# Performance work log

Measured on AMD Instinct MI355X. Metric: run time of the kernel, lower is better.

The kernel has to match this reference:

```python
import jax, jax.numpy as jnp
import numpy as np

N_NODES, N_EDGES, N_FEAT, N_CLASSES = 100000, 1600000, 50, 40
K_HOPS = 2


def setup_inputs() -> dict:
    key = jax.random.key(0)
    k1, k2, k3 = jax.random.split(key, 3)
    x = jax.random.normal(k1, (N_NODES, N_FEAT), dtype=jnp.float32)
    edge_index = jax.random.randint(k2, (2, N_EDGES), 0, N_NODES, dtype=jnp.int64)
    # Linear(num_features -> num_classes) params (PyG stores [out,in]; we use [in,out])
    W = jax.random.normal(k3, (N_FEAT, N_CLASSES), dtype=jnp.float32) * 0.05
    b = jnp.zeros((N_CLASSES,), dtype=jnp.float32)
    return {"x": x, "edge_index": edge_index, "W": W, "b": b}


def reference(x, edge_index, W, b):
    N = x.shape[0]
    # gcn_norm: add self-loops, symmetric normalization D^-1/2 (A+I) D^-1/2
    loop = jnp.arange(N, dtype=edge_index.dtype)
    row = jnp.concatenate([edge_index[0], loop])  # source nodes
    col = jnp.concatenate([edge_index[1], loop])  # target nodes
    deg = jax.ops.segment_sum(jnp.ones(row.shape[0], x.dtype), col, num_segments=N)
    deg_inv_sqrt = jnp.where(deg > 0, jax.lax.rsqrt(deg), 0.0)
    norm = deg_inv_sqrt[row] * deg_inv_sqrt[col]  # [E+N]

    # K-hop propagation: h <- scatter_add(norm * h[row] -> col)
    h = x
    for _ in range(K_HOPS):
        h = jax.ops.segment_sum(norm[:, None] * h[row], col, num_segments=N)

    logits = h @ W + b  # [N, C]
    return jax.nn.log_softmax(logits, axis=1)
```

## Files before the change

### kernel.cpp

```cpp
#include <hip/hip_runtime.h>
#include <math.h>

#define NFEAT 50
#define NCLS 40
#define TPBK 256
#define TPBK_SHIFT 8
#define EPB 4096
#define MAXNB 512

__device__ __forceinline__ float bf2f(unsigned short u) {
    return __uint_as_float(((unsigned)u) << 16);
}
__device__ __forceinline__ unsigned short f2bf(float f) {
    unsigned u = __float_as_uint(f);
    unsigned r = (u + 0x7FFFu + ((u >> 16) & 1u)) >> 16;
    return (unsigned short)r;
}


__global__ __launch_bounds__(1024) void k_bhist(const int* __restrict__ col, int E,
                                                int* __restrict__ bhist, int NB) {
    __shared__ int h[MAXNB];
    for (int i = threadIdx.x; i < NB; i += 1024) h[i] = 0;
    __syncthreads();
    int i0 = blockIdx.x * EPB;
    #pragma unroll
    for (int k = 0; k < EPB / 1024; k++) {
        int e = i0 + k * 1024 + threadIdx.x;
        if (e < E) atomicAdd(&h[col[e] >> TPBK_SHIFT], 1);
    }
    __syncthreads();
    for (int i = threadIdx.x; i < NB; i += 1024)
        if (h[i]) atomicAdd(&bhist[i], h[i]);
}


__global__ void k_bscan(const int* __restrict__ bhist, int* __restrict__ bbase,
                        int* __restrict__ gcur, int NB) {
    __shared__ int s[MAXNB];
    int t = threadIdx.x;
    int v = (t < NB) ? bhist[t] : 0;
    s[t] = v;
    __syncthreads();
    for (int off = 1; off < MAXNB; off <<= 1) {
        int a = (t >= off) ? s[t - off] : 0;
        __syncthreads();
        s[t] += a;
        __syncthreads();
    }
    if (t < NB) { int b = s[t] - v; bbase[t] = b; gcur[t] = b; }
}


__global__ __launch_bounds__(1024) void k_part(const int* __restrict__ ei, int E,
                                               int* __restrict__ gcur,
                                               int2* __restrict__ pairs, int NB) {
    __shared__ int h[MAXNB];
    __shared__ int base[MAXNB];
    int t = threadIdx.x;
    for (int i = t; i < NB; i += 1024) h[i] = 0;
    __syncthreads();
    int i0 = blockIdx.x * EPB;
    int r[EPB / 1024], c[EPB / 1024];
    #pragma unroll
    for (int k = 0; k < EPB / 1024; k++) {
        int e = i0 + k * 1024 + t;
        if (e < E) {
            r[k] = ei[e];
            c[k] = ei[E + e];
            atomicAdd(&h[c[k] >> TPBK_SHIFT], 1);
        } else c[k] = -1;
    }
    __syncthreads();
    for (int i = t; i < NB; i += 1024)
        base[i] = h[i] ? atomicAdd(&gcur[i], h[i]) : 0;
    __syncthreads();
    for (int i = t; i < NB; i += 1024) h[i] = 0;
    __syncthreads();
    #pragma unroll
    for (int k = 0; k < EPB / 1024; k++) {
        if (c[k] >= 0) {
            int bkt = c[k] >> TPBK_SHIFT;
            int p = base[bkt] + atomicAdd(&h[bkt], 1);
            pairs[p] = make_int2(r[k], c[k]);
        }
    }
}


__global__ __launch_bounds__(1024) void k_bucket(const int2* __restrict__ pairs,
                         const int* __restrict__ bbase,
                         const int* __restrict__ bhist, int* __restrict__ rows,
                         int* __restrict__ cnt, int* __restrict__ offs,
                         float* __restrict__ dis, const float* __restrict__ x,
                         unsigned short* __restrict__ xb, int N) {
    int b = blockIdx.x;
    int ebeg = bbase[b], m = bhist[b];
    int t0 = b << TPBK_SHIFT;
    __shared__ int h[TPBK];
    __shared__ int off[TPBK];
    __shared__ float diss[TPBK];
    __shared__ int wtot[4];
    int t = threadIdx.x;
    if (t < TPBK) h[t] = 0;
    __syncthreads();

    int2 pc[4]; bool ok[4];
    #pragma unroll
    for (int k = 0; k < 4; k++) {
        int i = t + k * 1024;
        ok[k] = i < m;
        if (ok[k]) {
            pc[k] = pairs[ebeg + i];
            atomicAdd(&h[pc[k].y - t0], 1);
        }
    }
    for (int i = 4096 + t; i < m; i += 1024)
        atomicAdd(&h[pairs[ebeg + i].y - t0], 1);
    __syncthreads();

    int v = 0, incl = 0;
    if (t < TPBK) {
        v = h[t];
        h[t] = 0;
        incl = v;
        int l = t & 63;
        #pragma unroll
        for (int d = 1; d < 64; d <<= 1) {
            int tmp = __shfl_up(incl, d);
            if (l >= d) incl += tmp;
        }
        if (l == 63) wtot[t >> 6] = incl;
    }
    __syncthreads();
    if (t < TPBK) {
        int pre = 0;
        #pragma unroll
        for (int w = 0; w < 3; w++) if ((t >> 6) > w) pre += wtot[w];
        int excl = pre + incl - v;
        off[t] = excl;
        int tg = t0 + t;
        float d = rsqrtf((float)(v + 1));
        diss[t] = d;
        if (tg < N) {
            cnt[tg] = v;
            offs[tg] = ebeg + excl;
            dis[tg] = d;
        }
    }
    __syncthreads();

    #pragma unroll
    for (int k = 0; k < 4; k++) {
        if (ok[k]) {
            int lt = pc[k].y - t0;
            int pos = off[lt] + atomicAdd(&h[lt], 1);
            rows[ebeg + pos] = pc[k].x;
        }
    }
    for (int i = 4096 + t; i < m; i += 1024) {
        int2 p = pairs[ebeg + i];
        int lt = p.y - t0;
        int pos = off[lt] + atomicAdd(&h[lt], 1);
        rows[ebeg + pos] = p.x;
    }

    int nmax = N - t0; if (nmax > TPBK) nmax = TPBK;
    for (int idx = t; idx < (nmax << 6); idx += 1024) {
        int nl = idx >> 6, f = idx & 63;
        int n = t0 + nl;
        float val = (f < NFEAT) ? x[(size_t)n * NFEAT + f] * diss[nl] : 0.f;
        xb[((size_t)n << 6) + f] = f2bf(val);
    }
}


__global__ void k_prop(const unsigned short* __restrict__ zin, unsigned short* __restrict__ zout,
                       const float* __restrict__ dis, const int* __restrict__ offs,
                       const int* __restrict__ cnt, const int* __restrict__ rows, int N) {
    int wid = (blockIdx.x * blockDim.x + threadIdx.x) >> 6;
    int lane = threadIdx.x & 63;
    if (wid >= N) return;
    int g = lane >> 4;
    int fl = (lane & 15) << 2;
    int beg = offs[wid], num = cnt[wid];

    float a0 = 0.f, a1 = 0.f, a2 = 0.f, a3 = 0.f;
    if (g == 0) {
        ushort4 s = *(const ushort4*)&zin[((size_t)wid << 6) + fl];
        a0 = bf2f(s.x); a1 = bf2f(s.y); a2 = bf2f(s.z); a3 = bf2f(s.w);
    }

    for (int j = 0; j < num; j += 16) {
        int i0 = j + (g << 2);
        int e0 = i0, e1 = i0 + 1, e2 = i0 + 2, e3 = i0 + 3;
        float m0 = e0 < num ? 1.f : 0.f;
        float m1 = e1 < num ? 1.f : 0.f;
        float m2 = e2 < num ? 1.f : 0.f;
        float m3 = e3 < num ? 1.f : 0.f;
        int c0 = e0 < num ? e0 : num - 1;
        int c1 = e1 < num ? e1 : num - 1;
        int c2 = e2 < num ? e2 : num - 1;
        int c3 = e3 < num ? e3 : num - 1;
        int r0 = rows[beg + c0];
        int r1 = rows[beg + c1];
        int r2 = rows[beg + c2];
        int r3 = rows[beg + c3];
        ushort4 v0 = *(const ushort4*)&zin[((size_t)r0 << 6) + fl];
        ushort4 v1 = *(const ushort4*)&zin[((size_t)r1 << 6) + fl];
        ushort4 v2 = *(const ushort4*)&zin[((size_t)r2 << 6) + fl];
        ushort4 v3 = *(const ushort4*)&zin[((size_t)r3 << 6) + fl];
        a0 = fmaf(m0, bf2f(v0.x), a0); a1 = fmaf(m0, bf2f(v0.y), a1);
        a2 = fmaf(m0, bf2f(v0.z), a2); a3 = fmaf(m0, bf2f(v0.w), a3);
        a0 = fmaf(m1, bf2f(v1.x), a0); a1 = fmaf(m1, bf2f(v1.y), a1);
        a2 = fmaf(m1, bf2f(v1.z), a2); a3 = fmaf(m1, bf2f(v1.w), a3);
        a0 = fmaf(m2, bf2f(v2.x), a0); a1 = fmaf(m2, bf2f(v2.y), a1);
        a2 = fmaf(m2, bf2f(v2.z), a2); a3 = fmaf(m2, bf2f(v2.w), a3);
        a0 = fmaf(m3, bf2f(v3.x), a0); a1 = fmaf(m3, bf2f(v3.y), a1);
        a2 = fmaf(m3, bf2f(v3.z), a2); a3 = fmaf(m3, bf2f(v3.w), a3);
    }

    a0 += __shfl_xor(a0, 16); a0 += __shfl_xor(a0, 32);
    a1 += __shfl_xor(a1, 16); a1 += __shfl_xor(a1, 32);
    a2 += __shfl_xor(a2, 16); a2 += __shfl_xor(a2, 32);
    a3 += __shfl_xor(a3, 16); a3 += __shfl_xor(a3, 32);

    float dn = dis[wid];
    float s2 = dn * dn;
    if (lane < 16) {
        ushort4 o;
        o.x = f2bf(a0 * s2); o.y = f2bf(a1 * s2);
        o.z = f2bf(a2 * s2); o.w = f2bf(a3 * s2);
        *(ushort4*)&zout[((size_t)wid << 6) + fl] = o;
    }
}


__global__ void k_head(const unsigned short* __restrict__ z2, const int* __restrict__ cnt,
                       const float* __restrict__ W, const float* __restrict__ b,
                       float* __restrict__ out, int N) {
    int n = blockIdx.x * blockDim.x + threadIdx.x;
    if (n >= N) return;
    float s = sqrtf((float)(cnt[n] + 1));
    float acc[NCLS];
    #pragma unroll
    for (int c = 0; c < NCLS; c++) acc[c] = b[c];
    for (int k = 0; k < NFEAT; k++) {
        float hk = bf2f(z2[((size_t)n << 6) + k]) * s;
        #pragma unroll
        for (int c = 0; c < NCLS; c++) acc[c] += hk * W[k * NCLS + c];
    }
    float m = acc[0];
    #pragma unroll
    for (int c = 1; c < NCLS; c++) m = fmaxf(m, acc[c]);
    float sum = 0.f;
    #pragma unroll
    for (int c = 0; c < NCLS; c++) sum += __expf(acc[c] - m);
    float l = __logf(sum) + m;
    #pragma unroll
    for (int c = 0; c < NCLS; c++) out[(size_t)n * NCLS + c] = acc[c] - l;
}


extern "C" void kernel_launch(void* const* d_in, const int* in_sizes, int n_in,
                              void* d_out, int out_size, void* d_ws, size_t ws_size,
                              hipStream_t stream) {
    const float* x = (const float*)d_in[0];
    const int* ei = (const int*)d_in[1];
    const float* W = (const float*)d_in[2];
    const float* b = (const float*)d_in[3];
    float* out = (float*)d_out;

    int N = in_sizes[0] / NFEAT;
    int E = in_sizes[1] / 2;
    int NB = (N + TPBK - 1) / TPBK;

    char* w = (char*)d_ws;
    auto alloc = [&](size_t bytes) { char* p = w; w += (bytes + 255) & ~(size_t)255; return p; };
    int*   bhist = (int*)  alloc((size_t)NB * 4);
    int*   bbase = (int*)  alloc((size_t)NB * 4);
    int*   gcur  = (int*)  alloc((size_t)NB * 4);
    int*   cnt   = (int*)  alloc((size_t)N * 4);
    int*   offs  = (int*)  alloc((size_t)N * 4);
    float* dis   = (float*)alloc((size_t)N * 4);
    int*   rows  = (int*)  alloc((size_t)E * 4);
    unsigned short* xb = (unsigned short*)alloc((size_t)N * 64 * 2);
    unsigned short* z1 = (unsigned short*)alloc((size_t)N * 64 * 2);
    char* uni = alloc((size_t)E * 8 > (size_t)N * 64 * 2 ? (size_t)E * 8 : (size_t)N * 64 * 2);
    int2* pairs = (int2*)uni;
    unsigned short* z2 = (unsigned short*)uni;

    hipMemsetAsync(bhist, 0, (size_t)NB * 4, stream);

    int pe = (E + EPB - 1) / EPB;
    k_bhist<<<pe, 1024, 0, stream>>>(ei + E, E, bhist, NB);
    k_bscan<<<1, MAXNB, 0, stream>>>(bhist, bbase, gcur, NB);
    k_part<<<pe, 1024, 0, stream>>>(ei, E, gcur, pairs, NB);
    k_bucket<<<NB, 1024, 0, stream>>>(pairs, bbase, bhist, rows, cnt, offs, dis, x, xb, N);

    int pb = (int)(((size_t)N * 64 + 255) / 256);
    k_prop<<<pb, 256, 0, stream>>>(xb, z1, dis, offs, cnt, rows, N);
    k_prop<<<pb, 256, 0, stream>>>(z1, z2, dis, offs, cnt, rows, N);

    k_head<<<(N + 255) / 256, 256, 0, stream>>>(z2, cnt, W, b, out, N);
}
```

Before: 163.7 us.

## Replace global atomic bucket cursors with per-block histogram scan; unmask full prop chunks

The bucket partition now stores a per-block histogram and does a column-wise exclusive scan across blocks in one kernel. Each partition block gets precomputed base offsets, which removes the memset, the global atomics on the bucket cursors and the second shared histogram pass in k_part. The prop kernel splits full 16-edge chunks into an unmasked loop with plain adds and keeps the masked path only for the tail. It also uses 32-bit index arithmetic. The single-block scan now walks all blocks serially per bucket (about 391 iterations), which could become a latency bottleneck.

```diff
diff --git a/kernel.cpp b/kernel.cpp
--- a/kernel.cpp
+++ b/kernel.cpp
@@ -19,7 +19,7 @@
 
 
 __global__ __launch_bounds__(1024) void k_bhist(const int* __restrict__ col, int E,
-                                                int* __restrict__ bhist, int NB) {
+                                                int* __restrict__ hist, int NB) {
     __shared__ int h[MAXNB];
     for (int i = threadIdx.x; i < NB; i += 1024) h[i] = 0;
     __syncthreads();
@@ -30,35 +30,57 @@
         if (e < E) atomicAdd(&h[col[e] >> TPBK_SHIFT], 1);
     }
     __syncthreads();
-    for (int i = threadIdx.x; i < NB; i += 1024)
-        if (h[i]) atomicAdd(&bhist[i], h[i]);
-}
-
-
-__global__ void k_bscan(const int* __restrict__ bhist, int* __restrict__ bbase,
-                        int* __restrict__ gcur, int NB) {
-    __shared__ int s[MAXNB];
+    int* row = hist + (size_t)blockIdx.x * NB;
+    for (int i = threadIdx.x; i < NB; i += 1024) row[i] = h[i];
+}
+
+
+__global__ __launch_bounds__(1024) void k_bscan(int* __restrict__ hist,
+                                                int* __restrict__ btot,
+                                                int* __restrict__ bbase,
+                                                int NB, int PE) {
     int t = threadIdx.x;
-    int v = (t < NB) ? bhist[t] : 0;
-    s[t] = v;
+    int s = 0;
+    if (t < NB) {
+        int p = 0;
+        for (; p + 4 <= PE; p += 4) {
+            s += hist[(size_t)p * NB + t] + hist[(size_t)(p + 1) * NB + t]
+               + hist[(size_t)(p + 2) * NB + t] + hist[(size_t)(p + 3) * NB + t];
+        }
+        for (; p < PE; p++) s += hist[(size_t)p * NB + t];
+        btot[t] = s;
+    }
+    __shared__ int sh[MAXNB];
+    if (t < MAXNB) sh[t] = (t < NB) ? s : 0;
     __syncthreads();
     for (int off = 1; off < MAXNB; off <<= 1) {
-        int a = (t >= off) ? s[t - off] : 0;
+        int a = (t < MAXNB && t >= off) ? sh[t - off] : 0;
         __syncthreads();
-        s[t] += a;
+        if (t < MAXNB) sh[t] += a;
         __syncthreads();
     }
-    if (t < NB) { int b = s[t] - v; bbase[t] = b; gcur[t] = b; }
+    if (t < NB) {
+        int base = sh[t] - s;
+        bbase[t] = base;
+        int run = base;
+        for (int p = 0; p < PE; p++) {
+            size_t idx = (size_t)p * NB + t;
+            int v = hist[idx];
+            hist[idx] = run;
+            run += v;
+        }
+    }
 }
 
 
 __global__ __launch_bounds__(1024) void k_part(const int* __restrict__ ei, int E,
-                                               int* __restrict__ gcur,
+                                               const int* __restrict__ hist,
                                                int2* __restrict__ pairs, int NB) {
     __shared__ int h[MAXNB];
     __shared__ int base[MAXNB];
     int t = threadIdx.x;
-    for (int i = t; i < NB; i += 1024) h[i] = 0;
+    const int* brow = hist + (size_t)blockIdx.x * NB;
+    for (int i = t; i < NB; i += 1024) { h[i] = 0; base[i] = brow[i]; }
     __syncthreads();
     int i0 = blockIdx.x * EPB;
     int r[EPB / 1024], c[EPB / 1024];
@@ -68,15 +90,8 @@
         if (e < E) {
             r[k] = ei[e];
             c[k] = ei[E + e];
-            atomicAdd(&h[c[k] >> TPBK_SHIFT], 1);
         } else c[k] = -1;
     }
-    __syncthreads();
-    for (int i = t; i < NB; i += 1024)
-        base[i] = h[i] ? atomicAdd(&gcur[i], h[i]) : 0;
-    __syncthreads();
-    for (int i = t; i < NB; i += 1024) h[i] = 0;
-    __syncthreads();
     #pragma unroll
     for (int k = 0; k < EPB / 1024; k++) {
         if (c[k] >= 0) {
@@ -90,12 +105,12 @@
 
 __global__ __launch_bounds__(1024) void k_bucket(const int2* __restrict__ pairs,
                          const int* __restrict__ bbase,
-                         const int* __restrict__ bhist, int* __restrict__ rows,
+                         const int* __restrict__ btot, int* __restrict__ rows,
                          int* __restrict__ cnt, int* __restrict__ offs,
                          float* __restrict__ dis, const float* __restrict__ x,
                          unsigned short* __restrict__ xb, int N) {
     int b = blockIdx.x;
-    int ebeg = bbase[b], m = bhist[b];
+    int ebeg = bbase[b], m = btot[b];
     int t0 = b << TPBK_SHIFT;
     __shared__ int h[TPBK];
     __shared__ int off[TPBK];
@@ -182,16 +197,31 @@
     int lane = threadIdx.x & 63;
     if (wid >= N) return;
     int g = lane >> 4;
-    int fl = (lane & 15) << 2;
+    unsigned fl = (lane & 15) << 2;
     int beg = offs[wid], num = cnt[wid];
 
-    float a0 = 0.f, a1 = 0.f, a2 = 0.f, a3 = 0.f;
-    if (g == 0) {
-        ushort4 s = *(const ushort4*)&zin[((size_t)wid << 6) + fl];
-        a0 = bf2f(s.x); a1 = bf2f(s.y); a2 = bf2f(s.z); a3 = bf2f(s.w);
-    }
-
-    for (int j = 0; j < num; j += 16) {
+    ushort4 sv = *(const ushort4*)&zin[((unsigned)wid << 6) + fl];
+    float keep = (g == 0) ? 1.f : 0.f;
+    float a0 = keep * bf2f(sv.x);
+    float a1 = keep * bf2f(sv.y);
+    float a2 = keep * bf2f(sv.z);
+    float a3 = keep * bf2f(sv.w);
+
+    int full = num & ~15;
+    int j = 0;
+    for (; j < full; j += 16) {
+        unsigned i0 = (unsigned)(beg + j) + ((unsigned)g << 2);
+        int r0 = rows[i0], r1 = rows[i0 + 1], r2 = rows[i0 + 2], r3 = rows[i0 + 3];
+        ushort4 v0 = *(const ushort4*)&zin[((unsigned)r0 << 6) + fl];
+        ushort4 v1 = *(const ushort4*)&zin[((unsigned)r1 << 6) + fl];
+        ushort4 v2 = *(const ushort4*)&zin[((unsigned)r2 << 6) + fl];
+        ushort4 v3 = *(const ushort4*)&zin[((unsigned)r3 << 6) + fl];
+        a0 += (bf2f(v0.x) + bf2f(v1.x)) + (bf2f(v2.x) + bf2f(v3.x));
+        a1 += (bf2f(v0.y) + bf2f(v1.y)) + (bf2f(v2.y) + bf2f(v3.y));
+        a2 += (bf2f(v0.z) + bf2f(v1.z)) + (bf2f(v2.z) + bf2f(v3.z));
+        a3 += (bf2f(v0.w) + bf2f(v1.w)) + (bf2f(v2.w) + bf2f(v3.w));
+    }
+    if (j < num) {
         int i0 = j + (g << 2);
         int e0 = i0, e1 = i0 + 1, e2 = i0 + 2, e3 = i0 + 3;
         float m0 = e0 < num ? 1.f : 0.f;
@@ -206,10 +236,10 @@
         int r1 = rows[beg + c1];
         int r2 = rows[beg + c2];
         int r3 = rows[beg + c3];
-        ushort4 v0 = *(const ushort4*)&zin[((size_t)r0 << 6) + fl];
-        ushort4 v1 = *(const ushort4*)&zin[((size_t)r1 << 6) + fl];
-        ushort4 v2 = *(const ushort4*)&zin[((size_t)r2 << 6) + fl];
-        ushort4 v3 = *(const ushort4*)&zin[((size_t)r3 << 6) + fl];
+        ushort4 v0 = *(const ushort4*)&zin[((unsigned)r0 << 6) + fl];
+        ushort4 v1 = *(const ushort4*)&zin[((unsigned)r1 << 6) + fl];
+        ushort4 v2 = *(const ushort4*)&zin[((unsigned)r2 << 6) + fl];
+        ushort4 v3 = *(const ushort4*)&zin[((unsigned)r3 << 6) + fl];
         a0 = fmaf(m0, bf2f(v0.x), a0); a1 = fmaf(m0, bf2f(v0.y), a1);
         a2 = fmaf(m0, bf2f(v0.z), a2); a3 = fmaf(m0, bf2f(v0.w), a3);
         a0 = fmaf(m1, bf2f(v1.x), a0); a1 = fmaf(m1, bf2f(v1.y), a1);
@@ -231,7 +261,7 @@
         ushort4 o;
         o.x = f2bf(a0 * s2); o.y = f2bf(a1 * s2);
         o.z = f2bf(a2 * s2); o.w = f2bf(a3 * s2);
-        *(ushort4*)&zout[((size_t)wid << 6) + fl] = o;
+        *(ushort4*)&zout[((unsigned)wid << 6) + fl] = o;
     }
 }
 
@@ -274,12 +304,13 @@
     int N = in_sizes[0] / NFEAT;
     int E = in_sizes[1] / 2;
     int NB = (N + TPBK - 1) / TPBK;
+    int pe = (E + EPB - 1) / EPB;
 
     char* w = (char*)d_ws;
     auto alloc = [&](size_t bytes) { char* p = w; w += (bytes + 255) & ~(size_t)255; return p; };
-    int*   bhist = (int*)  alloc((size_t)NB * 4);
+    int*   hist  = (int*)  alloc((size_t)pe * NB * 4);
+    int*   btot  = (int*)  alloc((size_t)NB * 4);
     int*   bbase = (int*)  alloc((size_t)NB * 4);
-    int*   gcur  = (int*)  alloc((size_t)NB * 4);
     int*   cnt   = (int*)  alloc((size_t)N * 4);
     int*   offs  = (int*)  alloc((size_t)N * 4);
     float* dis   = (float*)alloc((size_t)N * 4);
@@ -290,13 +321,10 @@
     int2* pairs = (int2*)uni;
     unsigned short* z2 = (unsigned short*)uni;
 
-    hipMemsetAsync(bhist, 0, (size_t)NB * 4, stream);
-
-    int pe = (E + EPB - 1) / EPB;
-    k_bhist<<<pe, 1024, 0, stream>>>(ei + E, E, bhist, NB);
-    k_bscan<<<1, MAXNB, 0, stream>>>(bhist, bbase, gcur, NB);
-    k_part<<<pe, 1024, 0, stream>>>(ei, E, gcur, pairs, NB);
-    k_bucket<<<NB, 1024, 0, stream>>>(pairs, bbase, bhist, rows, cnt, offs, dis, x, xb, N);
+    k_bhist<<<pe, 1024, 0, stream>>>(ei + E, E, hist, NB);
+    k_bscan<<<1, 1024, 0, stream>>>(hist, btot, bbase, NB, pe);
+    k_part<<<pe, 1024, 0, stream>>>(ei, E, hist, pairs, NB);
+    k_bucket<<<NB, 1024, 0, stream>>>(pairs, bbase, btot, rows, cnt, offs, dis, x, xb, N);
 
     int pb = (int)(((size_t)N * 64 + 255) / 256);
     k_prop<<<pb, 256, 0, stream>>>(xb, z1, dis, offs, cnt, rows, N);
```

New measurement: 202.1 us. 23.5% more time.
